# Performance work log

Hardware: AMD Instinct MI355X
Metric: run time of the kernel (lower is better)

The kernel has to match this reference:

```python
import jax, jax.numpy as jnp
import numpy as np

B, L, DIN = 16, 1024, 512
H, DH = 4, 128          # num_heads = 4, head_dim = in_features // 4
DEG = 16                # avg random in-degree (plus one self-loop per node)
NEG_SLOPE = 0.2         # DGL GATConv default leaky_relu slope


def setup_inputs() -> dict:
    key = jax.random.key(0)
    ks = jax.random.split(key, 8)
    N = B * L
    E = N * DEG
    src = jax.random.randint(ks[0], (E,), 0, N)
    dst = jax.random.randint(ks[1], (E,), 0, N)
    loops = jnp.arange(N)
    src = jnp.concatenate([src, loops])  # self-loops guarantee every dst has in-edges
    dst = jnp.concatenate([dst, loops])
    s = 1.0 / np.sqrt(DIN)
    text = jax.random.normal(ks[2], (B, L, DIN), jnp.float32)
    weight = jax.random.normal(ks[3], (DIN, DIN), jnp.float32) * s      # module's self.weight
    fc_w = jax.random.normal(ks[4], (DIN, H * DH), jnp.float32) * s     # GATConv fc (no bias)
    attn_l = jax.random.normal(ks[5], (H, DH), jnp.float32) * s
    attn_r = jax.random.normal(ks[6], (H, DH), jnp.float32) * s
    bias = jax.random.normal(ks[7], (DIN,), jnp.float32) * 0.01         # module's self.bias
    return {"text": text, "weight": weight, "fc_w": fc_w,
            "attn_l": attn_l, "attn_r": attn_r, "bias": bias,
            "src": src, "dst": dst}


def reference(text, weight, fc_w, attn_l, attn_r, bias, src, dst):
    b, l, d = text.shape
    N = b * l
    # outer linear projection
    hidden = jnp.einsum('bld,de->ble', text, weight)
    feat = hidden.reshape(N, d)
    # GATConv: fc projection to heads
    h = (feat @ fc_w).reshape(N, H, DH)                 # [N, H, DH]
    el = jnp.einsum('nhd,hd->nh', h, attn_l)            # [N, H]
    er = jnp.einsum('nhd,hd->nh', h, attn_r)            # [N, H]
    # edge attention logits (src contributes el, dst contributes er)
    e = jax.nn.leaky_relu(el[src] + er[dst], NEG_SLOPE)  # [E, H]
    # segment (per-destination) softmax, numerically stable
    emax = jax.ops.segment_max(e, dst, num_segments=N)   # [N, H]
    ex = jnp.exp(e - emax[dst])
    denom = jax.ops.segment_sum(ex, dst, num_segments=N)
    alpha = ex / denom[dst]                              # [E, H]
    # weighted message aggregation (scatter-add)
    m = h[src] * alpha[:, :, None]                       # [E, H, DH]
    out = jax.ops.segment_sum(m, dst, num_segments=N)    # [N, H, DH]
    return out.reshape(b, l, H * DH) + bias
```

## Files before the change

kernel.cpp:

```cpp
#include <hip/hip_runtime.h>
#include <stdint.h>

#define AS1 __attribute__((address_space(1)))
#define AS3 __attribute__((address_space(3)))

typedef __attribute__((ext_vector_type(8))) short short8;
typedef __attribute__((ext_vector_type(4))) float f32x4;

#define CAP 64
#define NSCAT 128

__device__ __forceinline__ short f2bf(float f) {
  union { float f; unsigned u; } v; v.f = f;
  unsigned r = v.u + 0x7fffu + ((v.u >> 16) & 1u);
  return (short)(r >> 16);
}
__device__ __forceinline__ float bf_lo(unsigned w) { union { unsigned u; float f; } v; v.u = w << 16;          return v.f; }
__device__ __forceinline__ float bf_hi(unsigned w) { union { unsigned u; float f; } v; v.u = w & 0xffff0000u;  return v.f; }

__global__ __launch_bounds__(256) void k_w2t(const float* __restrict__ W,
                                             const float* __restrict__ F,
                                             short* __restrict__ W2t,
                                             int* __restrict__ cnt) {
  const int tid = threadIdx.x;
  if (tid < 64) cnt[(blockIdx.y * 16 + blockIdx.x) * 64 + tid] = 0;

  __shared__ float sW[16][34];
  __shared__ float sF[16][34];
  const int dx = tid & 15, jy = tid >> 4;
  const int d0 = blockIdx.x * 32, j0 = blockIdx.y * 32;
  float a00 = 0.f, a01 = 0.f, a10 = 0.f, a11 = 0.f;
  const int wr = tid >> 3, wc2 = (tid & 7) * 2;
  const int fr = tid >> 4, fc2 = (tid & 15) * 2;
  for (int e0 = 0; e0 < 512; e0 += 16) {
    float2 wv = *(const float2*)&W[(size_t)(d0 + wr) * 512 + e0 + wc2];
    float2 fv = *(const float2*)&F[(size_t)(e0 + fr) * 512 + j0 + fc2];
    sW[wc2][wr] = wv.x; sW[wc2 + 1][wr] = wv.y;
    *(float2*)&sF[fr][fc2] = fv;
    __syncthreads();
#pragma unroll
    for (int e = 0; e < 16; ++e) {
      float2 w2 = *(const float2*)&sW[e][dx * 2];
      float2 f2 = *(const float2*)&sF[e][jy * 2];
      a00 += w2.x * f2.x; a01 += w2.x * f2.y;
      a10 += w2.y * f2.x; a11 += w2.y * f2.y;
    }
    __syncthreads();
  }
  short* o0 = W2t + (size_t)(j0 + jy * 2) * 512 + d0 + dx * 2;
  o0[0] = f2bf(a00); o0[1] = f2bf(a10);
  o0[512] = f2bf(a01); o0[513] = f2bf(a11);
}

#define GBM 32
#define GBK 64
__global__ __launch_bounds__(256) void k_gemm_scatter(const float* __restrict__ A32,
                                                      const short* __restrict__ Bt,
                                                      short* __restrict__ Cs,
                                                      float* __restrict__ el,
                                                      float* __restrict__ er,
                                                      const float* __restrict__ attn_l,
                                                      const float* __restrict__ attn_r,
                                                      const int* __restrict__ src,
                                                      const int* __restrict__ dst,
                                                      int* __restrict__ cnt,
                                                      int* __restrict__ bucket,
                                                      int E, int N) {
  __shared__ __align__(16) short sA[GBM * GBK];
  __shared__ __align__(16) short sB[512 * GBK];
  const int tid = threadIdx.x;

  if (blockIdx.x < NSCAT) {
    for (int e = blockIdx.x * 256 + tid; e < E; e += NSCAT * 256) {
      int d = dst[e];
      int p = atomicAdd(&cnt[d], 1);
      if (p < CAP) bucket[(size_t)d * CAP + p] = src[e];
    }
    return;
  }

  const int bx    = blockIdx.x - NSCAT;
  const int lane  = tid & 63;
  const int w     = tid >> 6;
  const int cc    = lane & 15;
  const int kslot = lane >> 4;
  const int bm0   = bx * GBM;

  f32x4 acc[2][8] = {};

  const int brow   = tid >> 3;
  const int bs_src = (tid & 7) ^ ((tid >> 3) & 7);
  const int bs_lin = tid & 7;
  const int arow    = tid >> 3;
  const int aslot_w = (tid & 7) ^ ((tid >> 3) & 7);

  for (int kt = 0; kt < 512 / GBK; ++kt) {
    const int kbase = kt * GBK;
#pragma unroll
    for (int k = 0; k < 16; ++k) {
      int row = brow + 32 * k;
      const short* gB = Bt + (size_t)row * 512 + kbase + bs_src * 8;
      short* lB = sB + row * GBK + bs_lin * 8;
      __builtin_amdgcn_global_load_lds((const AS1 void*)gB, (AS3 void*)lB, 16, 0, 0);
    }
    const float4* gA = (const float4*)(A32 + (size_t)(bm0 + arow) * 512 + kbase + (tid & 7) * 8);
    float4 a0 = gA[0], a1 = gA[1];
    short8 v;
    v[0] = f2bf(a0.x); v[1] = f2bf(a0.y); v[2] = f2bf(a0.z); v[3] = f2bf(a0.w);
    v[4] = f2bf(a1.x); v[5] = f2bf(a1.y); v[6] = f2bf(a1.z); v[7] = f2bf(a1.w);
    *(short8*)(sA + arow * GBK + aslot_w * 8) = v;
    __syncthreads();

#pragma unroll
    for (int ks = 0; ks < 2; ++ks) {
      const int g  = ks * 4 + kslot;
      const int sl = g ^ (cc & 7);
      short8 af0 = *(const short8*)(sA + (cc) * GBK + sl * 8);
      short8 af1 = *(const short8*)(sA + (16 + cc) * GBK + sl * 8);
#pragma unroll
      for (int j = 0; j < 8; ++j) {
        int row = w * 128 + j * 16 + cc;
        short8 bf = *(const short8*)(sB + row * GBK + sl * 8);
        acc[0][j] = __builtin_amdgcn_mfma_f32_16x16x32_bf16(af0, bf, acc[0][j], 0, 0, 0);
        acc[1][j] = __builtin_amdgcn_mfma_f32_16x16x32_bf16(af1, bf, acc[1][j], 0, 0, 0);
      }
    }
    __syncthreads();
  }

  const int r4 = (lane >> 4) * 4;
#pragma unroll
  for (int i = 0; i < 2; ++i)
#pragma unroll
    for (int j = 0; j < 8; ++j) {
      int cin = j * 16 + cc;
#pragma unroll
      for (int rg = 0; rg < 4; ++rg) {
        int gr = bm0 + i * 16 + r4 + rg;
        Cs[((size_t)w * N + gr) * 128 + cin] = f2bf(acc[i][j][rg]);
      }
    }
  float alv[8], arv[8];
#pragma unroll
  for (int j = 0; j < 8; ++j) {
    alv[j] = attn_l[w * 128 + j * 16 + cc];
    arv[j] = attn_r[w * 128 + j * 16 + cc];
  }
#pragma unroll
  for (int i = 0; i < 2; ++i)
#pragma unroll
    for (int rg = 0; rg < 4; ++rg) {
      float pl = 0.f, pr = 0.f;
#pragma unroll
      for (int j = 0; j < 8; ++j) {
        float vv = acc[i][j][rg];
        pl += vv * alv[j]; pr += vv * arv[j];
      }
#pragma unroll
      for (int d = 1; d < 16; d <<= 1) {
        pl += __shfl_xor(pl, d);
        pr += __shfl_xor(pr, d);
      }
      if (cc == 0) {
        int gr = bm0 + i * 16 + r4 + rg;
        el[gr * 4 + w] = pl;
        er[gr * 4 + w] = pr;
      }
    }
}

__global__ __launch_bounds__(256) void k_aggregate(const int* __restrict__ cnt, const int* __restrict__ bucket,
                                                   const float* __restrict__ el, const float* __restrict__ er,
                                                   const short* __restrict__ hs, const float* __restrict__ bias,
                                                   float* __restrict__ out, int N) {
  const int b    = blockIdx.x;
  const int s    = (b >> 1) & 3;
  const int nt   = (b >> 3) * 2 + (b & 1);
  const int nd   = nt * 4 + (threadIdx.x >> 6);
  const int lane = threadIdx.x & 63;
  const int g    = lane >> 4;
  const int cl   = lane & 15;

  int n = cnt[nd]; n = (n < CAP) ? n : CAP;
  const int* bk = bucket + (size_t)nd * CAP;

  int l   = (lane < n) ? lane : (n - 1);
  int idx = bk[l];
  float ern = er[nd * 4 + s];
  float x = el[idx * 4 + s] + ern;
  x = (x > 0.f) ? x : 0.2f * x;
  float wgt = (lane < n) ? __expf(x) : 0.f;
  float ssum = wgt;
#pragma unroll
  for (int d = 1; d < 64; d <<= 1) ssum += __shfl_xor(ssum, d);

  const short* hbase = hs + (size_t)s * N * 128;
  float acc[8];
#pragma unroll
  for (int j = 0; j < 8; ++j) acc[j] = 0.f;

  for (int base = 0; base < n; base += 8) {
    int e0 = base + g, e1 = base + 4 + g;
    int s0 = __shfl(idx, e0), s1 = __shfl(idx, e1);
    float w0 = __shfl(wgt, e0), w1 = __shfl(wgt, e1);
    uint4 v0 = ((const uint4*)(hbase + (size_t)s0 * 128))[cl];
    uint4 v1 = ((const uint4*)(hbase + (size_t)s1 * 128))[cl];
    acc[0] += w0 * bf_lo(v0.x) + w1 * bf_lo(v1.x);
    acc[1] += w0 * bf_hi(v0.x) + w1 * bf_hi(v1.x);
    acc[2] += w0 * bf_lo(v0.y) + w1 * bf_lo(v1.y);
    acc[3] += w0 * bf_hi(v0.y) + w1 * bf_hi(v1.y);
    acc[4] += w0 * bf_lo(v0.z) + w1 * bf_lo(v1.z);
    acc[5] += w0 * bf_hi(v0.z) + w1 * bf_hi(v1.z);
    acc[6] += w0 * bf_lo(v0.w) + w1 * bf_lo(v1.w);
    acc[7] += w0 * bf_hi(v0.w) + w1 * bf_hi(v1.w);
  }

#pragma unroll
  for (int d = 16; d < 64; d <<= 1) {
#pragma unroll
    for (int j = 0; j < 8; ++j) acc[j] += __shfl_xor(acc[j], d);
  }

  if (g == 0) {
    float inv = 1.f / ssum;
    int c0 = s * 128 + cl * 8;
    float4 b0 = *(const float4*)(bias + c0);
    float4 b1 = *(const float4*)(bias + c0 + 4);
    float4 o0, o1;
    o0.x = acc[0] * inv + b0.x; o0.y = acc[1] * inv + b0.y;
    o0.z = acc[2] * inv + b0.z; o0.w = acc[3] * inv + b0.w;
    o1.x = acc[4] * inv + b1.x; o1.y = acc[5] * inv + b1.y;
    o1.z = acc[6] * inv + b1.z; o1.w = acc[7] * inv + b1.w;
    float* op = out + (size_t)nd * 512 + c0;
    *(float4*)op = o0;
    *(float4*)(op + 4) = o1;
  }
}

extern "C" void kernel_launch(void* const* d_in, const int* in_sizes, int n_in,
                              void* d_out, int out_size, void* d_ws, size_t ws_size,
                              hipStream_t stream) {
  const float* text   = (const float*)d_in[0];
  const float* weight = (const float*)d_in[1];
  const float* fcw    = (const float*)d_in[2];
  const float* attn_l = (const float*)d_in[3];
  const float* attn_r = (const float*)d_in[4];
  const float* bias   = (const float*)d_in[5];
  const int*   src    = (const int*)d_in[6];
  const int*   dst    = (const int*)d_in[7];
  const int E = in_sizes[6];
  const int N = in_sizes[0] / 512;

  char* ws = (char*)d_ws;
  size_t o = 0;
  auto carve = [&](size_t bytes) { void* p = ws + o; o = (o + bytes + 255) & ~(size_t)255; return p; };
  short* w2t    = (short*)carve((size_t)512 * 512 * 2);
  short* hs     = (short*)carve((size_t)N * 512 * 2);
  float* el     = (float*)carve((size_t)N * 4 * 4);
  float* er     = (float*)carve((size_t)N * 4 * 4);
  int*   cnt    = (int*)carve((size_t)N * 4);
  int*   bucket = (int*)carve((size_t)N * CAP * 4);

  k_w2t<<<dim3(16, 16), 256, 0, stream>>>(weight, fcw, w2t, cnt);
  k_gemm_scatter<<<NSCAT + N / GBM, 256, 0, stream>>>(text, w2t, hs, el, er, attn_l, attn_r,
                                                      src, dst, cnt, bucket, E, N);
  k_aggregate<<<N * 4 / 4, 256, 0, stream>>>(cnt, bucket, el, er, hs, bias, (float*)d_out, N);
}
```

Before: 97.07 us.

## Retile fused GEMM to 128x128 blocks per head with 2x2 warp layout

The GEMM part of the fused kernel now uses 128x128 output tiles, one per (row block, head), with 4 waves arranged 2x2. Before, each block covered 32 rows across all 512 columns. This cuts the redundant LDS staging of the full 512-wide weight slice for every 32 rows and raises MFMA reuse per loaded fragment. The el/er reductions are combined across the two column waves through shared memory. The scatter blocks now come after the GEMM blocks in launch order, so they may start later. The 512-block grid is hardcoded and assumes N=16384.

After: 102.5 us. +5.6%, slower.

```diff
diff --git a/kernel.cpp b/kernel.cpp
--- a/kernel.cpp
+++ b/kernel.cpp
@@ -8,6 +8,7 @@
 typedef __attribute__((ext_vector_type(4))) float f32x4;
 
 #define CAP 64
+#define NGEMM 512
 #define NSCAT 128
 
 __device__ __forceinline__ short f2bf(float f) {
@@ -52,8 +53,6 @@
   o0[512] = f2bf(a01); o0[513] = f2bf(a11);
 }
 
-#define GBM 32
-#define GBK 64
 __global__ __launch_bounds__(256) void k_gemm_scatter(const float* __restrict__ A32,
                                                       const short* __restrict__ Bt,
                                                       short* __restrict__ Cs,
@@ -66,12 +65,9 @@
                                                       int* __restrict__ cnt,
                                                       int* __restrict__ bucket,
                                                       int E, int N) {
-  __shared__ __align__(16) short sA[GBM * GBK];
-  __shared__ __align__(16) short sB[512 * GBK];
   const int tid = threadIdx.x;
-
-  if (blockIdx.x < NSCAT) {
-    for (int e = blockIdx.x * 256 + tid; e < E; e += NSCAT * 256) {
+  if (blockIdx.x >= NGEMM) {
+    for (int e = (blockIdx.x - NGEMM) * 256 + tid; e < E; e += NSCAT * 256) {
       int d = dst[e];
       int p = atomicAdd(&cnt[d], 1);
       if (p < CAP) bucket[(size_t)d * CAP + p] = src[e];
@@ -79,82 +75,104 @@
     return;
   }
 
-  const int bx    = blockIdx.x - NSCAT;
-  const int lane  = tid & 63;
-  const int w     = tid >> 6;
-  const int cc    = lane & 15;
-  const int kslot = lane >> 4;
-  const int bm0   = bx * GBM;
-
-  f32x4 acc[2][8] = {};
-
-  const int brow   = tid >> 3;
-  const int bs_src = (tid & 7) ^ ((tid >> 3) & 7);
-  const int bs_lin = tid & 7;
-  const int arow    = tid >> 3;
-  const int aslot_w = (tid & 7) ^ ((tid >> 3) & 7);
-
-  for (int kt = 0; kt < 512 / GBK; ++kt) {
-    const int kbase = kt * GBK;
-#pragma unroll
-    for (int k = 0; k < 16; ++k) {
-      int row = brow + 32 * k;
-      const short* gB = Bt + (size_t)row * 512 + kbase + bs_src * 8;
-      short* lB = sB + row * GBK + bs_lin * 8;
+  __shared__ __align__(16) short sA[128 * 64];
+  __shared__ __align__(16) short sB[128 * 64];
+  __shared__ float sEl[128][2];
+  __shared__ float sEr[128][2];
+  const int bx   = blockIdx.x;
+  const int bm0  = (bx >> 2) * 128;
+  const int hh   = bx & 3;
+  const int bn0  = hh * 128;
+  const int lane = tid & 63;
+  const int wid  = tid >> 6;
+  const int wm   = wid >> 1;
+  const int wn   = wid & 1;
+  const int cc   = lane & 15;
+
+  f32x4 acc[4][4] = {};
+
+  const int srow  = tid >> 3;
+  const int sslot = (tid & 7) ^ (srow & 7);
+  const int lslot = tid & 7;
+  const int arow  = tid >> 1;
+  const int ahalf = tid & 1;
+
+  for (int kt = 0; kt < 8; ++kt) {
+    const int kbase = kt * 64;
+#pragma unroll
+    for (int r = 0; r < 4; ++r) {
+      int row = r * 32 + srow;
+      const short* gB = Bt + (size_t)(bn0 + row) * 512 + kbase + sslot * 8;
+      short* lB = sB + row * 64 + lslot * 8;
       __builtin_amdgcn_global_load_lds((const AS1 void*)gB, (AS3 void*)lB, 16, 0, 0);
     }
-    const float4* gA = (const float4*)(A32 + (size_t)(bm0 + arow) * 512 + kbase + (tid & 7) * 8);
-    float4 a0 = gA[0], a1 = gA[1];
-    short8 v;
-    v[0] = f2bf(a0.x); v[1] = f2bf(a0.y); v[2] = f2bf(a0.z); v[3] = f2bf(a0.w);
-    v[4] = f2bf(a1.x); v[5] = f2bf(a1.y); v[6] = f2bf(a1.z); v[7] = f2bf(a1.w);
-    *(short8*)(sA + arow * GBK + aslot_w * 8) = v;
-    __syncthreads();
-
+    const float4* gA = (const float4*)(A32 + (size_t)(bm0 + arow) * 512 + kbase + ahalf * 32);
+    float4 f[8];
+#pragma unroll
+    for (int s = 0; s < 8; ++s) f[s] = gA[s];
+#pragma unroll
+    for (int s = 0; s < 4; ++s) {
+      short8 v;
+      v[0] = f2bf(f[2 * s].x); v[1] = f2bf(f[2 * s].y);
+      v[2] = f2bf(f[2 * s].z); v[3] = f2bf(f[2 * s].w);
+      v[4] = f2bf(f[2 * s + 1].x); v[5] = f2bf(f[2 * s + 1].y);
+      v[6] = f2bf(f[2 * s + 1].z); v[7] = f2bf(f[2 * s + 1].w);
+      int slot = (ahalf * 4 + s) ^ (arow & 7);
+      *(short8*)(sA + arow * 64 + slot * 8) = v;
+    }
+    __syncthreads();
 #pragma unroll
     for (int ks = 0; ks < 2; ++ks) {
-      const int g  = ks * 4 + kslot;
-      const int sl = g ^ (cc & 7);
-      short8 af0 = *(const short8*)(sA + (cc) * GBK + sl * 8);
-      short8 af1 = *(const short8*)(sA + (16 + cc) * GBK + sl * 8);
-#pragma unroll
-      for (int j = 0; j < 8; ++j) {
-        int row = w * 128 + j * 16 + cc;
-        short8 bf = *(const short8*)(sB + row * GBK + sl * 8);
-        acc[0][j] = __builtin_amdgcn_mfma_f32_16x16x32_bf16(af0, bf, acc[0][j], 0, 0, 0);
-        acc[1][j] = __builtin_amdgcn_mfma_f32_16x16x32_bf16(af1, bf, acc[1][j], 0, 0, 0);
-      }
+      short8 af[4], bfr[4];
+#pragma unroll
+      for (int i = 0; i < 4; ++i) {
+        int row  = wm * 64 + i * 16 + cc;
+        int slot = (ks * 4 + (lane >> 4)) ^ (row & 7);
+        af[i] = *(const short8*)(sA + row * 64 + slot * 8);
+      }
+#pragma unroll
+      for (int j = 0; j < 4; ++j) {
+        int row  = wn * 64 + j * 16 + cc;
+        int slot = (ks * 4 + (lane >> 4)) ^ (row & 7);
+        bfr[j] = *(const short8*)(sB + row * 64 + slot * 8);
+      }
+#pragma unroll
+      for (int i = 0; i < 4; ++i)
+#pragma unroll
+        for (int j = 0; j < 4; ++j)
+          acc[i][j] = __builtin_amdgcn_mfma_f32_16x16x32_bf16(af[i], bfr[j], acc[i][j], 0, 0, 0);
     }
     __syncthreads();
   }
 
   const int r4 = (lane >> 4) * 4;
 #pragma unroll
-  for (int i = 0; i < 2; ++i)
-#pragma unroll
-    for (int j = 0; j < 8; ++j) {
-      int cin = j * 16 + cc;
+  for (int i = 0; i < 4; ++i)
+#pragma unroll
+    for (int j = 0; j < 4; ++j) {
+      int cin = wn * 64 + j * 16 + cc;
 #pragma unroll
       for (int rg = 0; rg < 4; ++rg) {
-        int gr = bm0 + i * 16 + r4 + rg;
-        Cs[((size_t)w * N + gr) * 128 + cin] = f2bf(acc[i][j][rg]);
-      }
-    }
-  float alv[8], arv[8];
-#pragma unroll
-  for (int j = 0; j < 8; ++j) {
-    alv[j] = attn_l[w * 128 + j * 16 + cc];
-    arv[j] = attn_r[w * 128 + j * 16 + cc];
-  }
-#pragma unroll
-  for (int i = 0; i < 2; ++i)
+        int gr = bm0 + wm * 64 + i * 16 + r4 + rg;
+        Cs[((size_t)hh * N + gr) * 128 + cin] = f2bf(acc[i][j][rg]);
+      }
+    }
+  float alv[4], arv[4];
+#pragma unroll
+  for (int j = 0; j < 4; ++j) {
+    int cl = wn * 64 + j * 16 + cc;
+    alv[j] = attn_l[hh * 128 + cl];
+    arv[j] = attn_r[hh * 128 + cl];
+  }
+#pragma unroll
+  for (int i = 0; i < 4; ++i)
 #pragma unroll
     for (int rg = 0; rg < 4; ++rg) {
       float pl = 0.f, pr = 0.f;
 #pragma unroll
-      for (int j = 0; j < 8; ++j) {
-        float vv = acc[i][j][rg];
-        pl += vv * alv[j]; pr += vv * arv[j];
+      for (int j = 0; j < 4; ++j) {
+        float v = acc[i][j][rg];
+        pl += v * alv[j]; pr += v * arv[j];
       }
 #pragma unroll
       for (int d = 1; d < 16; d <<= 1) {
@@ -162,11 +180,17 @@
         pr += __shfl_xor(pr, d);
       }
       if (cc == 0) {
-        int gr = bm0 + i * 16 + r4 + rg;
-        el[gr * 4 + w] = pl;
-        er[gr * 4 + w] = pr;
-      }
-    }
+        int row = wm * 64 + i * 16 + r4 + rg;
+        sEl[row][wn] = pl;
+        sEr[row][wn] = pr;
+      }
+    }
+  __syncthreads();
+  if (tid < 128) {
+    int gr = bm0 + tid;
+    el[gr * 4 + hh] = sEl[tid][0] + sEl[tid][1];
+    er[gr * 4 + hh] = sEr[tid][0] + sEr[tid][1];
+  }
 }
 
 __global__ __launch_bounds__(256) void k_aggregate(const int* __restrict__ cnt, const int* __restrict__ bucket,
@@ -262,7 +286,7 @@
   int*   bucket = (int*)carve((size_t)N * CAP * 4);
 
   k_w2t<<<dim3(16, 16), 256, 0, stream>>>(weight, fcw, w2t, cnt);
-  k_gemm_scatter<<<NSCAT + N / GBM, 256, 0, stream>>>(text, w2t, hs, el, er, attn_l, attn_r,
-                                                      src, dst, cnt, bucket, E, N);
+  k_gemm_scatter<<<NGEMM + NSCAT, 256, 0, stream>>>(text, w2t, hs, el, er, attn_l, attn_r,
+                                                    src, dst, cnt, bucket, E, N);
   k_aggregate<<<N * 4 / 4, 256, 0, stream>>>(cnt, bucket, el, er, hs, bias, (float*)d_out, N);
 }
```
